# Kernel optimization log

Measured on AMD Instinct MI355X. Metric: run time of the kernel, lower is better.

Reference implementation:

```python
import jax, jax.numpy as jnp
import numpy as np

L = 8192   # sequence length
B = 4      # batch
D = 512    # embed_dim
NDIM = 16  # EMA state dim
Z = 128    # shared q/k dim
W = 128    # attention window
MP = 256   # max relative positions
NEG = -50000.0  # TOKEN_SELF_ATTN_VALUE-style mask fill


def setup_inputs() -> dict:
    key = jax.random.key(0)
    ks = jax.random.split(key, 16)
    def tn(k, shp, std):  # truncated-normal-ish init (clipped normal)
        return jnp.clip(jax.random.normal(k, shp) * std, -2 * std, 2 * std)
    val = jnp.ones((NDIM, 1)).at[1::2].set(-1.0)  # MultiHeadEMA beta init pattern
    return {
        "x": jax.random.normal(ks[0], (L, B, D), dtype=jnp.float32),
        "delta": tn(ks[1], (D, NDIM, 1), 0.2),
        "alpha": tn(ks[2], (D, NDIM, 1), 0.2),
        "beta": tn(ks[3], (D, NDIM, 1), 0.02) + val,
        "gamma": jax.random.normal(ks[4], (D, NDIM)),
        "omega": jax.random.normal(ks[5], (D,)),
        "Wp": tn(ks[6], (D, 1), 0.02),      # LatentConfigurator weight_proj
        "bp": jnp.zeros((1,)),
        "temp": jnp.array([0.5 * np.log(D)], dtype=jnp.float32),  # log(sqrt(D))
        "Wz": tn(ks[7], (D, Z), 0.02),
        "qg": jax.random.normal(ks[8], (Z,)) * 0.02 + 1.0,
        "qb": jnp.zeros((Z,)),
        "kg": jax.random.normal(ks[9], (Z,)) * 0.02 + 1.0,
        "kb": jnp.zeros((Z,)),
        "Wv": tn(ks[10], (D, D), 0.02),
        "relb": tn(ks[11], (2 * MP - 1,), 0.02),  # FastRelativePositionalBias table
    }


def _rotary(t, cos, sin):
    # t: (B, L, Z); cos/sin: (L, Z//2). Complex rotation on interleaved pairs.
    t1, t2 = t[..., 0::2], t[..., 1::2]
    return jnp.stack([t1 * cos - t2 * sin, t1 * sin + t2 * cos], axis=-1).reshape(t.shape)


def _forward(x, delta, alpha, beta, gamma, omega, Wp, bp, temp, Wz, qg, qb, kg, kb, Wv, relb):
    scale = 1.0 / np.sqrt(NDIM)
    # ---- MultiHeadEMA: damped EMA as long convolution via FFT ----
    p = jax.nn.sigmoid(delta)                      # (D,N,1)
    a = jax.nn.sigmoid(alpha)
    logq = jnp.log1p(-(p * a))                     # log(1 - p*alpha)
    t = jnp.arange(L, dtype=jnp.float32)
    kern = (p * beta) * jnp.exp(logq * t)          # (D,N,L) Vandermonde kernel
    k1d = jnp.einsum('dnl,dn->dl', kern, gamma * scale)  # (D,L)
    xb = x.transpose(1, 2, 0)                      # (B,D,L)
    conv = jnp.fft.irfft(jnp.fft.rfft(xb, n=2 * L) * jnp.fft.rfft(k1d, n=2 * L), n=2 * L)[..., :L]
    mx = jax.nn.silu(conv.transpose(2, 0, 1) + x * omega)  # (L,B,D)
    # ---- LatentConfigurator: sigmoid token routing (proj_dim==1) ----
    pi = jax.nn.sigmoid((mx @ Wp + bp) / jnp.exp(temp))[..., 0].T  # (B,L)
    mxb = mx.transpose(1, 0, 2)                    # (B,L,D)
    sel = pi > 0.5
    idx = jnp.cumsum(sel.astype(jnp.int32), axis=1) * sel  # (B,L); 0 -> dropped slot
    counts = sel.sum(axis=1)                       # (B,)
    bi = jnp.arange(B)[:, None]
    # compress_seq: scatter selected tokens to compact prefix (slot 0 dropped)
    c = jnp.zeros((B, L + 1, D), mx.dtype).at[bi, idx].add(mxb * sel[..., None])[:, 1:]
    # ---- windowed attention over compressed tokens ----
    z = jax.nn.silu(c @ Wz)                        # (B,L,Z)
    freqs = 1.0 / (10000.0 ** (jnp.arange(0, Z, 2, dtype=jnp.float32) / Z))
    ang = jnp.arange(L, dtype=jnp.float32)[:, None] * freqs
    cos, sin = jnp.cos(ang), jnp.sin(ang)
    q = _rotary(z * qg + qb, cos, sin)
    kk = _rotary(z * kg + kb, cos, sin)
    v = jax.nn.silu(c @ Wv)                        # (B,L,D)
    n = L // W
    qw = q.reshape(B, n, W, Z)
    def look_around(tw):  # prepend previous window: (B,n,W,f) -> (B,n,2W,f)
        prev = jnp.pad(tw, ((0, 0), (1, 0), (0, 0), (0, 0)))[:, :-1]
        return jnp.concatenate([prev, tw], axis=2)
    kw = look_around(kk.reshape(B, n, W, Z))
    vw = look_around(v.reshape(B, n, W, D))
    base = (jnp.arange(n) * W)[:, None, None]
    qabs = base + jnp.arange(W)[None, :, None]         # (n,W,1)
    kabs = base + jnp.arange(-W, W)[None, None, :]     # (n,1,2W)
    mask = (kabs <= qabs) & (kabs >= 0) & (kabs[None] < counts[:, None, None, None])  # (B,n,W,2W)
    rel = jnp.arange(-W, W)[None, :] - jnp.arange(W)[:, None]   # (W,2W)
    bias = relb[jnp.clip(rel + MP - 1, 0, 2 * MP - 2)]          # (W,2W)
    scores = jnp.einsum('bnwz,bnkz->bnwk', qw, kw) / np.sqrt(Z) + bias
    attn = jax.nn.softmax(jnp.where(mask, scores, NEG), axis=-1)
    h = jnp.einsum('bnwk,bnkd->bnwd', attn, vw).reshape(B, L, D)
    # ---- extract: gather back to original positions, gate by pi ----
    hpad = jnp.concatenate([jnp.zeros((B, 1, D), h.dtype), h], axis=1)
    hsel = jnp.take_along_axis(hpad, idx[..., None], axis=1)    # (B,L,D)
    return x + (hsel * pi[..., None]).transpose(1, 0, 2)        # (L,B,D)


def reference(x, delta, alpha, beta, gamma, omega, Wp, bp, temp, Wz, qg, qb, kg, kb, Wv, relb):
    return _forward(x, delta, alpha, beta, gamma, omega, Wp, bp, temp, Wz, qg, qb, kg, kb, Wv, relb)
```

## Files before the change

### kernel.cpp

```cpp
#include <hip/hip_runtime.h>
#include <math.h>

constexpr int L = 8192;
constexpr int B = 4;
constexpr int D = 512;
constexpr int NDIM = 16;
constexpr int Z = 128;
constexpr float NEGF = -50000.0f;
constexpr int CCL = 64;
constexpr int NCH = L / CCL;

typedef short s16x8 __attribute__((ext_vector_type(8)));
typedef float f32x4 __attribute__((ext_vector_type(4)));

typedef __attribute__((address_space(1))) const void* as1cv;
typedef __attribute__((address_space(3))) void* as3v;

__device__ __forceinline__ void gld16(const void* g, void* l) {
  __builtin_amdgcn_global_load_lds((as1cv)g, (as3v)l, 16, 0, 0);
}

__device__ __forceinline__ unsigned short f2bf(float f) {
  unsigned u = __builtin_bit_cast(unsigned, f);
  u += 0x7fffu + ((u >> 16) & 1u);
  return (unsigned short)(u >> 16);
}

__global__ __launch_bounds__(256) void k_prep(const float* __restrict__ delta,
                                              const float* __restrict__ alpha,
                                              const float* __restrict__ beta,
                                              const float* __restrict__ gamma,
                                              double* __restrict__ qdn,
                                              double* __restrict__ cdn,
                                              double* __restrict__ rp1,
                                              double* __restrict__ rp2) {
  int i = blockIdx.x * 256 + threadIdx.x;
  if (i >= D * NDIM) return;
  double p = 1.0 / (1.0 + exp(-(double)delta[i]));
  double a = 1.0 / (1.0 + exp(-(double)alpha[i]));
  double q = 1.0 - p * a;
  qdn[i] = q;
  cdn[i] = p * (double)beta[i] * (double)gamma[i] * 0.25;
  double q2 = q * q, q4 = q2 * q2, q8 = q4 * q4;
  double q16 = q8 * q8, q32 = q16 * q16, q64 = q32 * q32;
  rp1[i] = q64;
  rp2[i] = q64 * q64;
}

__global__ __launch_bounds__(256) void k_convA(const float* __restrict__ x,
                                               const double* __restrict__ qdn,
                                               float* __restrict__ E) {
  int bx = blockIdx.x;
  int tile = bx & 31, dg = (bx >> 5) & 7, b = bx >> 8;
  int d = threadIdx.x & 63, cl = threadIdx.x >> 6;
  int dgl = dg * 64 + d;
  int t = tile * 4 + cl;
  double q[NDIM], s[NDIM];
#pragma unroll
  for (int n = 0; n < NDIM; ++n) { q[n] = qdn[dgl * NDIM + n]; s[n] = 0.0; }
  const float* xp = x + ((size_t)(t * CCL) * B + b) * D + dgl;
#pragma unroll 4
  for (int i = 0; i < CCL; ++i) {
    double xv = (double)xp[(size_t)i * (B * D)];
#pragma unroll
    for (int n = 0; n < NDIM; ++n) s[n] = fma(q[n], s[n], xv);
  }
  float* eb = E + ((size_t)(b * NCH + t) * NDIM) * 512 + dgl;
#pragma unroll
  for (int n = 0; n < NDIM; ++n) eb[(size_t)n * 512] = (float)s[n];
}

__global__ __launch_bounds__(256) void k_convC(const float* __restrict__ x,
                                               const float* __restrict__ omega,
                                               const double* __restrict__ qdn,
                                               const double* __restrict__ cdn,
                                               const double* __restrict__ rp1,
                                               const double* __restrict__ rp2,
                                               const float* __restrict__ E,
                                               float* __restrict__ mx) {
  int bx = blockIdx.x;
  int tile = bx & 31, dg = (bx >> 5) & 7, b = bx >> 8;
  int d = threadIdx.x & 63, cl = threadIdx.x >> 6;
  int dgl = dg * 64 + d;
  int t = tile * 4 + cl;
  double q[NDIM], c[NDIM], s[NDIM];
#pragma unroll
  for (int n = 0; n < NDIM; ++n) {
    q[n] = qdn[dgl * NDIM + n];
    c[n] = cdn[dgl * NDIM + n];
    s[n] = 0.0;
  }
  if (t >= 1) {
    const float* e1 = E + ((size_t)(b * NCH + t - 1) * NDIM) * 512 + dgl;
#pragma unroll
    for (int n = 0; n < NDIM; ++n) s[n] = (double)e1[(size_t)n * 512];
  }
  if (t >= 2) {
    const float* e2 = E + ((size_t)(b * NCH + t - 2) * NDIM) * 512 + dgl;
#pragma unroll
    for (int n = 0; n < NDIM; ++n) s[n] = fma(rp1[dgl * NDIM + n], (double)e2[(size_t)n * 512], s[n]);
  }
  if (t >= 3) {
    const float* e3 = E + ((size_t)(b * NCH + t - 3) * NDIM) * 512 + dgl;
#pragma unroll
    for (int n = 0; n < NDIM; ++n) s[n] = fma(rp2[dgl * NDIM + n], (double)e3[(size_t)n * 512], s[n]);
  }
  double om = (double)omega[dgl];
  const float* xp = x + ((size_t)(t * CCL) * B + b) * D + dgl;
  float* mp = mx + ((size_t)b * L + t * CCL) * 512 + dgl;
#pragma unroll 4
  for (int i = 0; i < CCL; ++i) {
    double xv = (double)xp[(size_t)i * (B * D)];
#pragma unroll
    for (int n = 0; n < NDIM; ++n) s[n] = fma(q[n], s[n], xv);
    double p0 = c[0] * s[0], p1 = c[1] * s[1], p2 = c[2] * s[2], p3 = c[3] * s[3];
    p0 = fma(c[4], s[4], p0);  p1 = fma(c[5], s[5], p1);
    p2 = fma(c[6], s[6], p2);  p3 = fma(c[7], s[7], p3);
    p0 = fma(c[8], s[8], p0);  p1 = fma(c[9], s[9], p1);
    p2 = fma(c[10], s[10], p2); p3 = fma(c[11], s[11], p3);
    p0 = fma(c[12], s[12], p0); p1 = fma(c[13], s[13], p1);
    p2 = fma(c[14], s[14], p2); p3 = fma(c[15], s[15], p3);
    double conv = (p0 + p1) + (p2 + p3);
    float m = (float)(conv + xv * om);
    float sg = 1.0f / (1.0f + expf(-m));
    mp[(size_t)i * 512] = m * sg;
  }
}

__global__ __launch_bounds__(256) void k_logit(const float* __restrict__ mx,
                                               const float* __restrict__ Wp,
                                               const float* __restrict__ bp,
                                               const float* __restrict__ temp,
                                               float* __restrict__ pi,
                                               int* __restrict__ selb) {
  int rid = blockIdx.x * 4 + (threadIdx.x >> 6);
  int lane = threadIdx.x & 63;
  const float* row = mx + (size_t)rid * D;
  double acc = 0.0;
#pragma unroll
  for (int i = 0; i < D / 64; ++i)
    acc += (double)row[lane + 64 * i] * (double)Wp[lane + 64 * i];
  for (int off = 32; off; off >>= 1) acc += __shfl_down(acc, off, 64);
  if (lane == 0) {
    double logit = acc + (double)bp[0];
    double scl = logit / exp((double)temp[0]);
    pi[rid] = (float)(1.0 / (1.0 + exp(-scl)));
    selb[rid] = (logit > 0.0) ? 1 : 0;
  }
}

__global__ __launch_bounds__(256) void k_scan(const int* __restrict__ selb,
                                              int* __restrict__ idx,
                                              int* __restrict__ src,
                                              int* __restrict__ counts) {
  int b = blockIdx.x;
  int t = threadIdx.x;
  __shared__ int part[256];
  const int PER = L / 256;
  int base = b * L + t * PER;
  int loc[PER];
  int cnt = 0;
#pragma unroll
  for (int i = 0; i < PER; ++i) { loc[i] = selb[base + i]; cnt += loc[i]; }
  part[t] = cnt;
  __syncthreads();
  for (int off = 1; off < 256; off <<= 1) {
    int v = (t >= off) ? part[t - off] : 0;
    __syncthreads();
    part[t] += v;
    __syncthreads();
  }
  int run = (t == 0) ? 0 : part[t - 1];
#pragma unroll
  for (int i = 0; i < PER; ++i) {
    int sflag = loc[i];
    run += sflag;
    idx[base + i] = sflag ? run : 0;
    if (sflag) src[b * L + run - 1] = t * PER + i;
  }
  if (t == 255) counts[b] = part[255];
}

__global__ __launch_bounds__(256) void k_buildc(const float* __restrict__ mx,
                                                const int* __restrict__ src,
                                                const int* __restrict__ counts,
                                                unsigned short* __restrict__ c) {
  int row = blockIdx.x * 4 + (threadIdx.x >> 6);
  int lane = threadIdx.x & 63;
  int b = row >> 13;
  int j = row & (L - 1);
  float4 v0 = {0.f, 0.f, 0.f, 0.f}, v1 = v0;
  if (j < counts[b]) {
    const float4* mr = (const float4*)(mx + ((size_t)b * L + src[row]) * D);
    v0 = mr[lane * 2];
    v1 = mr[lane * 2 + 1];
  }
  s16x8 o;
  o[0] = (short)f2bf(v0.x); o[1] = (short)f2bf(v0.y);
  o[2] = (short)f2bf(v0.z); o[3] = (short)f2bf(v0.w);
  o[4] = (short)f2bf(v1.x); o[5] = (short)f2bf(v1.y);
  o[6] = (short)f2bf(v1.z); o[7] = (short)f2bf(v1.w);
  *(s16x8*)(c + (size_t)row * D + lane * 8) = o;
}

__global__ __launch_bounds__(256) void k_wt(const float* __restrict__ Wm,
                                            unsigned short* __restrict__ Wt, int N) {
  int idx = blockIdx.x * 256 + threadIdx.x;
  int n = idx >> 9, kk = idx & 511;
  Wt[idx] = f2bf(Wm[(size_t)kk * N + n]);
}

__global__ __launch_bounds__(256) void k_gemm_mfma(const unsigned short* __restrict__ A,
                                                   const unsigned short* __restrict__ Bt,
                                                   float* __restrict__ outF,
                                                   unsigned short* __restrict__ outT,
                                                   int N, int mode) {
  __shared__ char As[16384];
  __shared__ char Bs[16384];
  int tid = threadIdx.x;
  int w = tid >> 6, l = tid & 63;
  int m0 = blockIdx.x * 128, n0 = blockIdx.y * 128;
  int wr = w >> 1, wc = w & 1;
  f32x4 acc[4][4];
  f32x4 zz = {0.f, 0.f, 0.f, 0.f};
#pragma unroll
  for (int mi = 0; mi < 4; ++mi)
#pragma unroll
    for (int ni = 0; ni < 4; ++ni) acc[mi][ni] = zz;

  for (int k0 = 0; k0 < 512; k0 += 64) {
#pragma unroll
    for (int ld = 0; ld < 4; ++ld) {
      int li = w * 4 + ld;
      int row = li * 8 + (l >> 3);
      int col = (((l & 7) ^ (row & 7)) << 3);
      gld16(A + (size_t)(m0 + row) * 512 + k0 + col, As + li * 1024);
      gld16(Bt + (size_t)(n0 + row) * 512 + k0 + col, Bs + li * 1024);
    }
    __syncthreads();
    s16x8 af[4][2], bfr[4][2];
#pragma unroll
    for (int kh = 0; kh < 2; ++kh) {
#pragma unroll
      for (int mi = 0; mi < 4; ++mi) {
        int row = wr * 64 + mi * 16 + (l & 15);
        int byte = row * 128 + ((kh * 64 + ((l >> 4) * 16)) ^ ((row & 7) << 4));
        af[mi][kh] = *(const s16x8*)(As + byte);
      }
#pragma unroll
      for (int ni = 0; ni < 4; ++ni) {
        int row = wc * 64 + ni * 16 + (l & 15);
        int byte = row * 128 + ((kh * 64 + ((l >> 4) * 16)) ^ ((row & 7) << 4));
        bfr[ni][kh] = *(const s16x8*)(Bs + byte);
      }
    }
#pragma unroll
    for (int kh = 0; kh < 2; ++kh)
#pragma unroll
      for (int mi = 0; mi < 4; ++mi)
#pragma unroll
        for (int ni = 0; ni < 4; ++ni)
          acc[mi][ni] = __builtin_amdgcn_mfma_f32_16x16x32_bf16(af[mi][kh], bfr[ni][kh], acc[mi][ni], 0, 0, 0);
    __syncthreads();
  }
#pragma unroll
  for (int mi = 0; mi < 4; ++mi)
#pragma unroll
    for (int ni = 0; ni < 4; ++ni)
#pragma unroll
      for (int r = 0; r < 4; ++r) {
        float vv = acc[mi][ni][r];
        vv = vv / (1.0f + __expf(-vv));
        int mrow = m0 + wr * 64 + mi * 16 + (l >> 4) * 4 + r;
        int ncol = n0 + wc * 64 + ni * 16 + (l & 15);
        if (mode == 0) {
          outF[(size_t)mrow * N + ncol] = vv;
        } else {
          int b = mrow >> 13, j = mrow & 8191;
          outT[((size_t)(b * 512 + ncol)) * 8192 + j] = f2bf(vv);
        }
      }
}

__global__ __launch_bounds__(256) void k_rot(const float* __restrict__ z,
                                             const float* __restrict__ qg,
                                             const float* __restrict__ qb,
                                             const float* __restrict__ kg,
                                             const float* __restrict__ kb,
                                             unsigned short* __restrict__ qo,
                                             unsigned short* __restrict__ ko) {
  int tid = blockIdx.x * 256 + threadIdx.x;
  int i = tid & 63;
  int row = tid >> 6;
  int j = row & (L - 1);
  double freq = exp(((double)(-2 * i) / 128.0) * log(10000.0));
  float angf = (float)j * (float)freq;
  double sa, ca;
  sincos((double)angf, &sa, &ca);
  float cc = (float)ca, ss = (float)sa;
  size_t base = (size_t)row * Z + 2 * i;
  float z1 = z[base], z2 = z[base + 1];
  float q1 = z1 * qg[2 * i] + qb[2 * i], q2 = z2 * qg[2 * i + 1] + qb[2 * i + 1];
  float k1 = z1 * kg[2 * i] + kb[2 * i], k2 = z2 * kg[2 * i + 1] + kb[2 * i + 1];
  qo[base]     = f2bf(q1 * cc - q2 * ss);
  qo[base + 1] = f2bf(q1 * ss + q2 * cc);
  ko[base]     = f2bf(k1 * cc - k2 * ss);
  ko[base + 1] = f2bf(k1 * ss + k2 * cc);
}

__global__ __launch_bounds__(512) void k_attn_mfma(const unsigned short* __restrict__ q,
                                                   const unsigned short* __restrict__ k,
                                                   const unsigned short* __restrict__ vT,
                                                   const float* __restrict__ relb,
                                                   const int* __restrict__ counts,
                                                   float* __restrict__ h) {
  __shared__ char smem[131072];
  char* Qs = smem;
  char* Ks = smem + 32768;
  char* Ps = smem;
  char* Vs = smem + 65536;
  int tid = threadIdx.x, w = tid >> 6, l = tid & 63;
  int n = blockIdx.x & 63, b = blockIdx.x >> 6;
  int cnt = counts[b];
  int q0 = n * 128, kbase = q0 - 128;
  const size_t rowb = (size_t)b * L;

#pragma unroll
  for (int ld = 0; ld < 4; ++ld) {
    int li = w * 4 + ld;
    int row = li * 4 + (l >> 4);
    int colb = ((l & 15) * 16) ^ ((row & 7) << 4);
    gld16((const char*)(q + (rowb + q0 + row) * Z) + colb, Qs + li * 1024);
  }
#pragma unroll
  for (int ld = 0; ld < 8; ++ld) {
    int li = w * 8 + ld;
    int row = li * 4 + (l >> 4);
    int jk = kbase + row; if (jk < 0) jk = 0;
    int colb = ((l & 15) * 16) ^ ((row & 7) << 4);
    gld16((const char*)(k + (rowb + jk) * Z) + colb, Ks + li * 1024);
  }
  __syncthreads();

  int m0 = w * 16;
  f32x4 s[16];
  f32x4 zz = {0.f, 0.f, 0.f, 0.f};
#pragma unroll
  for (int ni = 0; ni < 16; ++ni) s[ni] = zz;
  s16x8 aq[4];
#pragma unroll
  for (int ks = 0; ks < 4; ++ks) {
    int row = m0 + (l & 15);
    int byte = row * 256 + ((ks * 64 + ((l >> 4) * 16)) ^ ((row & 7) << 4));
    aq[ks] = *(const s16x8*)(Qs + byte);
  }
#pragma unroll
  for (int ni = 0; ni < 16; ++ni) {
    int row = ni * 16 + (l & 15);
    int rb = row * 256, sw = (row & 7) << 4;
#pragma unroll
    for (int ks = 0; ks < 4; ++ks) {
      s16x8 bk = *(const s16x8*)(Ks + rb + ((ks * 64 + ((l >> 4) * 16)) ^ sw));
      s[ni] = __builtin_amdgcn_mfma_f32_16x16x32_bf16(aq[ks], bk, s[ni], 0, 0, 0);
    }
  }
  __syncthreads();

  auto stageV = [&](int nc) {
#pragma unroll
    for (int ld = 0; ld < 8; ++ld) {
      int li = w * 8 + ld;
      int row = li * 2 + (l >> 5);
      int colb = ((l & 31) * 16) ^ ((row & 7) << 4);
      int j = kbase + (colb >> 1);
      if (j < 0) j = 0;
      gld16((const char*)(vT + ((size_t)(b * 512 + nc * 128 + row)) * L + j), Vs + li * 1024);
    }
  };
  stageV(0);

  int rgrp = (l >> 4) * 4;
  float mxr[4] = {-3e38f, -3e38f, -3e38f, -3e38f};
#pragma unroll
  for (int ni = 0; ni < 16; ++ni) {
    int col = ni * 16 + (l & 15);
    int kabs = kbase + col;
#pragma unroll
    for (int r = 0; r < 4; ++r) {
      int ww = m0 + rgrp + r;
      bool valid = (kabs >= 0) && (kabs <= q0 + ww) && (kabs < cnt);
      float vv = valid ? (s[ni][r] * 0.08838834764831845f + relb[col + 127 - ww]) : NEGF;
      s[ni][r] = vv;
      mxr[r] = fmaxf(mxr[r], vv);
    }
  }
#pragma unroll
  for (int r = 0; r < 4; ++r)
    for (int off = 1; off < 16; off <<= 1)
      mxr[r] = fmaxf(mxr[r], __shfl_xor(mxr[r], off, 64));
  float smr[4] = {0.f, 0.f, 0.f, 0.f};
#pragma unroll
  for (int ni = 0; ni < 16; ++ni)
#pragma unroll
    for (int r = 0; r < 4; ++r) {
      float p = __expf(s[ni][r] - mxr[r]);
      s[ni][r] = p;
      smr[r] += p;
    }
#pragma unroll
  for (int r = 0; r < 4; ++r) {
    for (int off = 1; off < 16; off <<= 1) smr[r] += __shfl_xor(smr[r], off, 64);
    smr[r] = 1.0f / smr[r];
  }
#pragma unroll
  for (int ni = 0; ni < 16; ++ni) {
    int colb2 = (ni * 16 + (l & 15)) * 2;
#pragma unroll
    for (int r = 0; r < 4; ++r) {
      int row = m0 + rgrp + r;
      *(unsigned short*)(Ps + row * 512 + (colb2 ^ ((row & 7) << 4))) = f2bf(s[ni][r] * smr[r]);
    }
  }
  __syncthreads();

  for (int nc = 0; nc < 4; ++nc) {
    if (nc) {
      __syncthreads();
      stageV(nc);
      __syncthreads();
    }
    f32x4 o[8];
#pragma unroll
    for (int ni = 0; ni < 8; ++ni) o[ni] = zz;
    int prow = m0 + (l & 15);
    int psw = (prow & 7) << 4;
#pragma unroll
    for (int kt = 0; kt < 4; ++kt) {
      s16x8 pa0 = *(const s16x8*)(Ps + prow * 512 + ((kt * 128 + ((l >> 4) * 16)) ^ psw));
      s16x8 pa1 = *(const s16x8*)(Ps + prow * 512 + ((kt * 128 + 64 + ((l >> 4) * 16)) ^ psw));
#pragma unroll
      for (int ni = 0; ni < 8; ++ni) {
        int vrow = ni * 16 + (l & 15);
        int vsw = (vrow & 7) << 4;
        s16x8 vb0 = *(const s16x8*)(Vs + vrow * 512 + ((kt * 128 + ((l >> 4) * 16)) ^ vsw));
        s16x8 vb1 = *(const s16x8*)(Vs + vrow * 512 + ((kt * 128 + 64 + ((l >> 4) * 16)) ^ vsw));
        o[ni] = __builtin_amdgcn_mfma_f32_16x16x32_bf16(pa0, vb0, o[ni], 0, 0, 0);
        o[ni] = __builtin_amdgcn_mfma_f32_16x16x32_bf16(pa1, vb1, o[ni], 0, 0, 0);
      }
    }
#pragma unroll
    for (int ni = 0; ni < 8; ++ni)
#pragma unroll
      for (int r = 0; r < 4; ++r)
        h[(rowb + q0 + m0 + rgrp + r) * 512 + nc * 128 + ni * 16 + (l & 15)] = o[ni][r];
  }
}

__global__ __launch_bounds__(256) void k_final(const float* __restrict__ x,
                                               const float* __restrict__ h,
                                               const float* __restrict__ pi,
                                               const int* __restrict__ idx,
                                               float* __restrict__ out) {
  int e4 = blockIdx.x * 256 + threadIdx.x;
  int dq = e4 & 127;
  int rem = e4 >> 7;
  int b = rem & 3;
  int l = rem >> 2;
  float4 xv = ((const float4*)x)[e4];
  int ix = idx[(b << 13) + l];
  if (ix > 0) {
    float pv = pi[(b << 13) + l];
    float4 hv = ((const float4*)(h + ((size_t)(b << 13) + ix - 1) * 512))[dq];
    xv.x += hv.x * pv; xv.y += hv.y * pv;
    xv.z += hv.z * pv; xv.w += hv.w * pv;
  }
  ((float4*)out)[e4] = xv;
}

extern "C" void kernel_launch(void* const* d_in, const int* in_sizes, int n_in,
                              void* d_out, int out_size, void* d_ws, size_t ws_size,
                              hipStream_t stream) {
  const float* x     = (const float*)d_in[0];
  const float* delta = (const float*)d_in[1];
  const float* alpha = (const float*)d_in[2];
  const float* beta  = (const float*)d_in[3];
  const float* gamma = (const float*)d_in[4];
  const float* omega = (const float*)d_in[5];
  const float* Wp    = (const float*)d_in[6];
  const float* bp    = (const float*)d_in[7];
  const float* temp  = (const float*)d_in[8];
  const float* Wz    = (const float*)d_in[9];
  const float* qg    = (const float*)d_in[10];
  const float* qb    = (const float*)d_in[11];
  const float* kg    = (const float*)d_in[12];
  const float* kb    = (const float*)d_in[13];
  const float* Wv    = (const float*)d_in[14];
  const float* relb  = (const float*)d_in[15];
  (void)in_sizes; (void)n_in; (void)out_size; (void)ws_size;

  char* wsb = (char*)d_ws;
  size_t o = 0;
  auto alloc = [&](size_t bytes) {
    char* p = wsb + o;
    o += (bytes + 255) & ~(size_t)255;
    return p;
  };
  float* mxv           = (float*)alloc((size_t)B * L * D * 4);
  char*  eAndCb        = alloc((size_t)B * L * D * 2);
  float* Ebuf          = (float*)eAndCb;
  unsigned short* cb   = (unsigned short*)eAndCb;
  float* zb            = (float*)alloc((size_t)B * L * Z * 4);
  unsigned short* qb2  = (unsigned short*)alloc((size_t)B * L * Z * 2);
  unsigned short* kb2  = (unsigned short*)alloc((size_t)B * L * Z * 2);
  unsigned short* vTb  = (unsigned short*)alloc((size_t)B * D * L * 2);
  unsigned short* wzt  = (unsigned short*)alloc((size_t)Z * 512 * 2);
  unsigned short* wvt  = (unsigned short*)alloc((size_t)D * 512 * 2);
  float* pib = (float*)alloc((size_t)B * L * 4);
  int* selb  = (int*)alloc((size_t)B * L * 4);
  int* idx   = (int*)alloc((size_t)B * L * 4);
  int* src   = (int*)alloc((size_t)B * L * 4);
  int* cnt   = (int*)alloc(256);
  double* qdn = (double*)alloc((size_t)D * NDIM * 8);
  double* cdn = (double*)alloc((size_t)D * NDIM * 8);
  double* rp1 = (double*)alloc((size_t)D * NDIM * 8);
  double* rp2 = (double*)alloc((size_t)D * NDIM * 8);

  k_prep<<<(D * NDIM + 255) / 256, 256, 0, stream>>>(delta, alpha, beta, gamma, qdn, cdn, rp1, rp2);
  k_convA<<<B * 8 * 32, 256, 0, stream>>>(x, qdn, Ebuf);
  k_convC<<<B * 8 * 32, 256, 0, stream>>>(x, omega, qdn, cdn, rp1, rp2, Ebuf, mxv);
  k_logit<<<B * L / 4, 256, 0, stream>>>(mxv, Wp, bp, temp, pib, selb);
  k_scan<<<B, 256, 0, stream>>>(selb, idx, src, cnt);
  k_buildc<<<B * L / 4, 256, 0, stream>>>(mxv, src, cnt, cb);
  k_wt<<<Z * 512 / 256, 256, 0, stream>>>(Wz, wzt, Z);
  k_wt<<<D * 512 / 256, 256, 0, stream>>>(Wv, wvt, D);
  k_gemm_mfma<<<dim3(256, 1), 256, 0, stream>>>(cb, wzt, zb, vTb, Z, 0);
  k_gemm_mfma<<<dim3(256, 4), 256, 0, stream>>>(cb, wvt, zb, vTb, D, 1);
  k_rot<<<B * L * (Z / 2) / 256, 256, 0, stream>>>(zb, qg, qb, kg, kb, qb2, kb2);
  k_attn_mfma<<<B * 64, 512, 0, stream>>>(qb2, kb2, vTb, relb, cnt, mxv);
  k_final<<<(int)((size_t)L * B * D / 4 / 256), 256, 0, stream>>>(x, mxv, pib, idx, (float*)d_out);
}
```

Baseline: 270.5 us.

## Run EMA convolution in fp32, fuse logit dot, store bf16 mx, fix near-zero logits

The EMA chunked convolution moves from double to single precision, and the Wp projection dot product is fused into the convolution kernel through per-64-channel partial sums. This drops the separate logit pass over the fp32 mx buffer, and mx is now written as bf16, so buildc only gathers rows. Rows whose logit lands near zero are flagged and recomputed in double precision by small fix kernels, to keep the selection decision faithful. The cost is two extra tiny launches, an atomic counter, and reduced precision in the pi values and in mx.

```diff
diff --git a/kernel.cpp b/kernel.cpp
--- a/kernel.cpp
+++ b/kernel.cpp
@@ -9,6 +9,7 @@
 constexpr float NEGF = -50000.0f;
 constexpr int CCL = 64;
 constexpr int NCH = L / CCL;
+constexpr int FMAX = 64;
 
 typedef short s16x8 __attribute__((ext_vector_type(8)));
 typedef float f32x4 __attribute__((ext_vector_type(4)));
@@ -33,120 +34,212 @@
                                               double* __restrict__ qdn,
                                               double* __restrict__ cdn,
                                               double* __restrict__ rp1,
-                                              double* __restrict__ rp2) {
+                                              double* __restrict__ rp2,
+                                              float* __restrict__ qf,
+                                              float* __restrict__ cf,
+                                              float* __restrict__ r1f,
+                                              float* __restrict__ r2f,
+                                              int* __restrict__ fcnt) {
   int i = blockIdx.x * 256 + threadIdx.x;
+  if (i == 0) *fcnt = 0;
   if (i >= D * NDIM) return;
   double p = 1.0 / (1.0 + exp(-(double)delta[i]));
   double a = 1.0 / (1.0 + exp(-(double)alpha[i]));
   double q = 1.0 - p * a;
-  qdn[i] = q;
-  cdn[i] = p * (double)beta[i] * (double)gamma[i] * 0.25;
+  double c = p * (double)beta[i] * (double)gamma[i] * 0.25;
+  qdn[i] = q; cdn[i] = c;
   double q2 = q * q, q4 = q2 * q2, q8 = q4 * q4;
   double q16 = q8 * q8, q32 = q16 * q16, q64 = q32 * q32;
   rp1[i] = q64;
   rp2[i] = q64 * q64;
+  qf[i] = (float)q; cf[i] = (float)c;
+  r1f[i] = (float)q64; r2f[i] = (float)(q64 * q64);
 }
 
 __global__ __launch_bounds__(256) void k_convA(const float* __restrict__ x,
-                                               const double* __restrict__ qdn,
+                                               const float* __restrict__ qf,
                                                float* __restrict__ E) {
   int bx = blockIdx.x;
   int tile = bx & 31, dg = (bx >> 5) & 7, b = bx >> 8;
-  int d = threadIdx.x & 63, cl = threadIdx.x >> 6;
-  int dgl = dg * 64 + d;
+  int dl = threadIdx.x & 63, cl = threadIdx.x >> 6;
+  int dgl = dg * 64 + dl;
   int t = tile * 4 + cl;
-  double q[NDIM], s[NDIM];
-#pragma unroll
-  for (int n = 0; n < NDIM; ++n) { q[n] = qdn[dgl * NDIM + n]; s[n] = 0.0; }
+  float q[NDIM], s[NDIM];
+#pragma unroll
+  for (int n = 0; n < NDIM; ++n) { q[n] = qf[dgl * NDIM + n]; s[n] = 0.f; }
   const float* xp = x + ((size_t)(t * CCL) * B + b) * D + dgl;
 #pragma unroll 4
   for (int i = 0; i < CCL; ++i) {
-    double xv = (double)xp[(size_t)i * (B * D)];
-#pragma unroll
-    for (int n = 0; n < NDIM; ++n) s[n] = fma(q[n], s[n], xv);
+    float xv = xp[i * (B * D)];
+#pragma unroll
+    for (int n = 0; n < NDIM; ++n) s[n] = fmaf(q[n], s[n], xv);
   }
   float* eb = E + ((size_t)(b * NCH + t) * NDIM) * 512 + dgl;
 #pragma unroll
-  for (int n = 0; n < NDIM; ++n) eb[(size_t)n * 512] = (float)s[n];
+  for (int n = 0; n < NDIM; ++n) eb[(size_t)n * 512] = s[n];
 }
 
 __global__ __launch_bounds__(256) void k_convC(const float* __restrict__ x,
                                                const float* __restrict__ omega,
-                                               const double* __restrict__ qdn,
-                                               const double* __restrict__ cdn,
-                                               const double* __restrict__ rp1,
-                                               const double* __restrict__ rp2,
+                                               const float* __restrict__ qf,
+                                               const float* __restrict__ cf,
+                                               const float* __restrict__ r1f,
+                                               const float* __restrict__ r2f,
                                                const float* __restrict__ E,
-                                               float* __restrict__ mx) {
+                                               const float* __restrict__ Wp,
+                                               unsigned short* __restrict__ mxb,
+                                               float* __restrict__ pdot) {
   int bx = blockIdx.x;
   int tile = bx & 31, dg = (bx >> 5) & 7, b = bx >> 8;
-  int d = threadIdx.x & 63, cl = threadIdx.x >> 6;
-  int dgl = dg * 64 + d;
+  int dl = threadIdx.x & 63, cl = threadIdx.x >> 6;
+  int dgl = dg * 64 + dl;
   int t = tile * 4 + cl;
-  double q[NDIM], c[NDIM], s[NDIM];
+  float q[NDIM], c[NDIM], s[NDIM];
 #pragma unroll
   for (int n = 0; n < NDIM; ++n) {
-    q[n] = qdn[dgl * NDIM + n];
-    c[n] = cdn[dgl * NDIM + n];
-    s[n] = 0.0;
+    q[n] = qf[dgl * NDIM + n];
+    c[n] = cf[dgl * NDIM + n];
+    s[n] = 0.f;
   }
   if (t >= 1) {
     const float* e1 = E + ((size_t)(b * NCH + t - 1) * NDIM) * 512 + dgl;
 #pragma unroll
-    for (int n = 0; n < NDIM; ++n) s[n] = (double)e1[(size_t)n * 512];
+    for (int n = 0; n < NDIM; ++n) s[n] = e1[(size_t)n * 512];
   }
   if (t >= 2) {
     const float* e2 = E + ((size_t)(b * NCH + t - 2) * NDIM) * 512 + dgl;
 #pragma unroll
-    for (int n = 0; n < NDIM; ++n) s[n] = fma(rp1[dgl * NDIM + n], (double)e2[(size_t)n * 512], s[n]);
+    for (int n = 0; n < NDIM; ++n) s[n] = fmaf(r1f[dgl * NDIM + n], e2[(size_t)n * 512], s[n]);
   }
   if (t >= 3) {
     const float* e3 = E + ((size_t)(b * NCH + t - 3) * NDIM) * 512 + dgl;
 #pragma unroll
-    for (int n = 0; n < NDIM; ++n) s[n] = fma(rp2[dgl * NDIM + n], (double)e3[(size_t)n * 512], s[n]);
-  }
-  double om = (double)omega[dgl];
+    for (int n = 0; n < NDIM; ++n) s[n] = fmaf(r2f[dgl * NDIM + n], e3[(size_t)n * 512], s[n]);
+  }
+  float om = omega[dgl];
+  float wp = Wp[dgl];
   const float* xp = x + ((size_t)(t * CCL) * B + b) * D + dgl;
-  float* mp = mx + ((size_t)b * L + t * CCL) * 512 + dgl;
-#pragma unroll 4
+  unsigned short* mp = mxb + ((size_t)b * L + t * CCL) * 512 + dgl;
+  float* pp = pdot + ((size_t)(b * L + t * CCL)) * 8 + dg;
   for (int i = 0; i < CCL; ++i) {
-    double xv = (double)xp[(size_t)i * (B * D)];
-#pragma unroll
-    for (int n = 0; n < NDIM; ++n) s[n] = fma(q[n], s[n], xv);
-    double p0 = c[0] * s[0], p1 = c[1] * s[1], p2 = c[2] * s[2], p3 = c[3] * s[3];
-    p0 = fma(c[4], s[4], p0);  p1 = fma(c[5], s[5], p1);
-    p2 = fma(c[6], s[6], p2);  p3 = fma(c[7], s[7], p3);
-    p0 = fma(c[8], s[8], p0);  p1 = fma(c[9], s[9], p1);
-    p2 = fma(c[10], s[10], p2); p3 = fma(c[11], s[11], p3);
-    p0 = fma(c[12], s[12], p0); p1 = fma(c[13], s[13], p1);
-    p2 = fma(c[14], s[14], p2); p3 = fma(c[15], s[15], p3);
-    double conv = (p0 + p1) + (p2 + p3);
-    float m = (float)(conv + xv * om);
-    float sg = 1.0f / (1.0f + expf(-m));
-    mp[(size_t)i * 512] = m * sg;
-  }
-}
-
-__global__ __launch_bounds__(256) void k_logit(const float* __restrict__ mx,
-                                               const float* __restrict__ Wp,
-                                               const float* __restrict__ bp,
-                                               const float* __restrict__ temp,
-                                               float* __restrict__ pi,
-                                               int* __restrict__ selb) {
-  int rid = blockIdx.x * 4 + (threadIdx.x >> 6);
-  int lane = threadIdx.x & 63;
-  const float* row = mx + (size_t)rid * D;
+    float xv = xp[i * (B * D)];
+#pragma unroll
+    for (int n = 0; n < NDIM; ++n) s[n] = fmaf(q[n], s[n], xv);
+    float p0 = c[0] * s[0], p1 = c[1] * s[1], p2 = c[2] * s[2], p3 = c[3] * s[3];
+    p0 = fmaf(c[4], s[4], p0);  p1 = fmaf(c[5], s[5], p1);
+    p2 = fmaf(c[6], s[6], p2);  p3 = fmaf(c[7], s[7], p3);
+    p0 = fmaf(c[8], s[8], p0);  p1 = fmaf(c[9], s[9], p1);
+    p2 = fmaf(c[10], s[10], p2); p3 = fmaf(c[11], s[11], p3);
+    p0 = fmaf(c[12], s[12], p0); p1 = fmaf(c[13], s[13], p1);
+    p2 = fmaf(c[14], s[14], p2); p3 = fmaf(c[15], s[15], p3);
+    float conv = (p0 + p1) + (p2 + p3);
+    float m = fmaf(xv, om, conv);
+    float v = m / (1.0f + __expf(-m));
+    mp[(size_t)i * 512] = f2bf(v);
+    float pd = v * wp;
+#pragma unroll
+    for (int off = 32; off; off >>= 1) pd += __shfl_down(pd, off, 64);
+    if (dl == 0) pp[(size_t)i * 8] = pd;
+  }
+}
+
+__global__ __launch_bounds__(256) void k_logitc(const float* __restrict__ pdot,
+                                                const float* __restrict__ bp,
+                                                const float* __restrict__ temp,
+                                                float* __restrict__ pi,
+                                                int* __restrict__ selb,
+                                                int* __restrict__ fcnt,
+                                                int* __restrict__ flags) {
+  int rid = blockIdx.x * 256 + threadIdx.x;
+  const float* pr = pdot + (size_t)rid * 8;
   double acc = 0.0;
 #pragma unroll
-  for (int i = 0; i < D / 64; ++i)
-    acc += (double)row[lane + 64 * i] * (double)Wp[lane + 64 * i];
-  for (int off = 32; off; off >>= 1) acc += __shfl_down(acc, off, 64);
-  if (lane == 0) {
-    double logit = acc + (double)bp[0];
-    double scl = logit / exp((double)temp[0]);
-    pi[rid] = (float)(1.0 / (1.0 + exp(-scl)));
-    selb[rid] = (logit > 0.0) ? 1 : 0;
-  }
+  for (int j = 0; j < 8; ++j) acc += (double)pr[j];
+  double logit = acc + (double)bp[0];
+  pi[rid] = (float)(1.0 / (1.0 + exp(-logit / exp((double)temp[0]))));
+  selb[rid] = (logit > 0.0) ? 1 : 0;
+  if (fabs(logit) < 1e-4) {
+    int slot = atomicAdd(fcnt, 1);
+    if (slot < FMAX) flags[slot] = rid;
+  }
+}
+
+__global__ __launch_bounds__(256) void k_fix(const int* __restrict__ fcnt,
+                                             const int* __restrict__ flags,
+                                             const float* __restrict__ x,
+                                             const double* __restrict__ qdn,
+                                             const double* __restrict__ cdn,
+                                             const double* __restrict__ rp1,
+                                             const double* __restrict__ rp2,
+                                             const float* __restrict__ omega,
+                                             const float* __restrict__ Wp,
+                                             double* __restrict__ pfix) {
+  int nb = blockIdx.x;
+  int fi = nb >> 3, dblk = nb & 7;
+  int count = *fcnt; if (count > FMAX) count = FMAX;
+  if (fi >= count) return;
+  int rid = flags[fi];
+  int b = rid >> 13, l = rid & (L - 1);
+  int t = l >> 6, io = l & 63;
+  int sub = threadIdx.x >> 6, dl = threadIdx.x & 63;
+  int d = dblk * 64 + dl;
+  double q[NDIM], s[NDIM];
+#pragma unroll
+  for (int n = 0; n < NDIM; ++n) { q[n] = qdn[d * NDIM + n]; s[n] = 0.0; }
+  int c0 = (sub < 3) ? (t - 3 + sub) : t;
+  int steps = (sub < 3) ? 64 : (io + 1);
+  if (c0 >= 0) {
+    const float* xp = x + ((size_t)(c0 * CCL) * B + b) * D + d;
+    for (int i = 0; i < steps; ++i) {
+      double xv = (double)xp[(size_t)i * (B * D)];
+#pragma unroll
+      for (int n = 0; n < NDIM; ++n) s[n] = fma(q[n], s[n], xv);
+    }
+  }
+  __shared__ double Esm[4][64][NDIM];
+#pragma unroll
+  for (int n = 0; n < NDIM; ++n) Esm[sub][dl][n] = s[n];
+  __syncthreads();
+  if (sub == 3) {
+    double sfin[NDIM];
+#pragma unroll
+    for (int n = 0; n < NDIM; ++n) {
+      double base = q[n], r = 1.0;
+      int e = io + 1;
+      while (e) { if (e & 1) r *= base; base *= base; e >>= 1; }
+      double S = Esm[2][dl][n] + rp1[d * NDIM + n] * Esm[1][dl][n] + rp2[d * NDIM + n] * Esm[0][dl][n];
+      sfin[n] = Esm[3][dl][n] + r * S;
+    }
+    double conv = 0.0;
+#pragma unroll
+    for (int n = 0; n < NDIM; ++n) conv = fma(cdn[d * NDIM + n], sfin[n], conv);
+    double xv = (double)x[((size_t)l * B + b) * D + d];
+    double m = conv + xv * (double)omega[d];
+    double mxd = m / (1.0 + exp(-m));
+    double v = mxd * (double)Wp[d];
+#pragma unroll
+    for (int off = 32; off; off >>= 1) v += __shfl_down(v, off, 64);
+    if (dl == 0) pfix[fi * 8 + dblk] = v;
+  }
+}
+
+__global__ __launch_bounds__(64) void k_fix2(const int* __restrict__ fcnt,
+                                             const int* __restrict__ flags,
+                                             const double* __restrict__ pfix,
+                                             const float* __restrict__ bp,
+                                             const float* __restrict__ temp,
+                                             float* __restrict__ pi,
+                                             int* __restrict__ selb) {
+  int fi = threadIdx.x;
+  int count = *fcnt; if (count > FMAX) count = FMAX;
+  if (fi >= count) return;
+  double s = 0.0;
+#pragma unroll
+  for (int j = 0; j < 8; ++j) s += pfix[fi * 8 + j];
+  double logit = s + (double)bp[0];
+  int rid = flags[fi];
+  selb[rid] = (logit > 0.0) ? 1 : 0;
+  pi[rid] = (float)(1.0 / (1.0 + exp(-logit / exp((double)temp[0]))));
 }
 
 __global__ __launch_bounds__(256) void k_scan(const int* __restrict__ selb,
@@ -181,7 +274,7 @@
   if (t == 255) counts[b] = part[255];
 }
 
-__global__ __launch_bounds__(256) void k_buildc(const float* __restrict__ mx,
+__global__ __launch_bounds__(256) void k_buildc(const unsigned short* __restrict__ mxb,
                                                 const int* __restrict__ src,
                                                 const int* __restrict__ counts,
                                                 unsigned short* __restrict__ c) {
@@ -189,17 +282,9 @@
   int lane = threadIdx.x & 63;
   int b = row >> 13;
   int j = row & (L - 1);
-  float4 v0 = {0.f, 0.f, 0.f, 0.f}, v1 = v0;
-  if (j < counts[b]) {
-    const float4* mr = (const float4*)(mx + ((size_t)b * L + src[row]) * D);
-    v0 = mr[lane * 2];
-    v1 = mr[lane * 2 + 1];
-  }
-  s16x8 o;
-  o[0] = (short)f2bf(v0.x); o[1] = (short)f2bf(v0.y);
-  o[2] = (short)f2bf(v0.z); o[3] = (short)f2bf(v0.w);
-  o[4] = (short)f2bf(v1.x); o[5] = (short)f2bf(v1.y);
-  o[6] = (short)f2bf(v1.z); o[7] = (short)f2bf(v1.w);
+  s16x8 o = {0, 0, 0, 0, 0, 0, 0, 0};
+  if (j < counts[b])
+    o = *(const s16x8*)(mxb + ((size_t)b * L + src[row]) * 512 + lane * 8);
   *(s16x8*)(c + (size_t)row * D + lane * 8) = o;
 }
 
@@ -505,7 +590,8 @@
     o += (bytes + 255) & ~(size_t)255;
     return p;
   };
-  float* mxv           = (float*)alloc((size_t)B * L * D * 4);
+  float* hbuf          = (float*)alloc((size_t)B * L * D * 4);
+  unsigned short* mxb  = (unsigned short*)hbuf;
   char*  eAndCb        = alloc((size_t)B * L * D * 2);
   float* Ebuf          = (float*)eAndCb;
   unsigned short* cb   = (unsigned short*)eAndCb;
@@ -515,27 +601,38 @@
   unsigned short* vTb  = (unsigned short*)alloc((size_t)B * D * L * 2);
   unsigned short* wzt  = (unsigned short*)alloc((size_t)Z * 512 * 2);
   unsigned short* wvt  = (unsigned short*)alloc((size_t)D * 512 * 2);
-  float* pib = (float*)alloc((size_t)B * L * 4);
-  int* selb  = (int*)alloc((size_t)B * L * 4);
-  int* idx   = (int*)alloc((size_t)B * L * 4);
-  int* src   = (int*)alloc((size_t)B * L * 4);
-  int* cnt   = (int*)alloc(256);
+  float* pdot = (float*)alloc((size_t)B * L * 8 * 4);
+  float* pib  = (float*)alloc((size_t)B * L * 4);
+  int* selb   = (int*)alloc((size_t)B * L * 4);
+  int* idx    = (int*)alloc((size_t)B * L * 4);
+  int* src    = (int*)alloc((size_t)B * L * 4);
+  int* cnt    = (int*)alloc(256);
   double* qdn = (double*)alloc((size_t)D * NDIM * 8);
   double* cdn = (double*)alloc((size_t)D * NDIM * 8);
   double* rp1 = (double*)alloc((size_t)D * NDIM * 8);
   double* rp2 = (double*)alloc((size_t)D * NDIM * 8);
-
-  k_prep<<<(D * NDIM + 255) / 256, 256, 0, stream>>>(delta, alpha, beta, gamma, qdn, cdn, rp1, rp2);
-  k_convA<<<B * 8 * 32, 256, 0, stream>>>(x, qdn, Ebuf);
-  k_convC<<<B * 8 * 32, 256, 0, stream>>>(x, omega, qdn, cdn, rp1, rp2, Ebuf, mxv);
-  k_logit<<<B * L / 4, 256, 0, stream>>>(mxv, Wp, bp, temp, pib, selb);
+  float* qf   = (float*)alloc((size_t)D * NDIM * 4);
+  float* cf   = (float*)alloc((size_t)D * NDIM * 4);
+  float* r1f  = (float*)alloc((size_t)D * NDIM * 4);
+  float* r2f  = (float*)alloc((size_t)D * NDIM * 4);
+  int* fcnt   = (int*)alloc(256);
+  int* flags  = (int*)alloc(FMAX * 4);
+  double* pfix = (double*)alloc((size_t)FMAX * 8 * 8);
+
+  k_prep<<<(D * NDIM + 255) / 256, 256, 0, stream>>>(delta, alpha, beta, gamma,
+                                                     qdn, cdn, rp1, rp2, qf, cf, r1f, r2f, fcnt);
+  k_convA<<<B * 8 * 32, 256, 0, stream>>>(x, qf, Ebuf);
+  k_convC<<<B * 8 * 32, 256, 0, stream>>>(x, omega, qf, cf, r1f, r2f, Ebuf, Wp, mxb, pdot);
+  k_logitc<<<B * L / 256, 256, 0, stream>>>(pdot, bp, temp, pib, selb, fcnt, flags);
+  k_fix<<<FMAX * 8, 256, 0, stream>>>(fcnt, flags, x, qdn, cdn, rp1, rp2, omega, Wp, pfix);
+  k_fix2<<<1, 64, 0, stream>>>(fcnt, flags, pfix, bp, temp, pib, selb);
   k_scan<<<B, 256, 0, stream>>>(selb, idx, src, cnt);
-  k_buildc<<<B * L / 4, 256, 0, stream>>>(mxv, src, cnt, cb);
+  k_buildc<<<B * L / 4, 256, 0, stream>>>(mxb, src, cnt, cb);
   k_wt<<<Z * 512 / 256, 256, 0, stream>>>(Wz, wzt, Z);
   k_wt<<<D * 512 / 256, 256, 0, stream>>>(Wv, wvt, D);
   k_gemm_mfma<<<dim3(256, 1), 256, 0, stream>>>(cb, wzt, zb, vTb, Z, 0);
   k_gemm_mfma<<<dim3(256, 4), 256, 0, stream>>>(cb, wvt, zb, vTb, D, 1);
   k_rot<<<B * L * (Z / 2) / 256, 256, 0, stream>>>(zb, qg, qb, kg, kb, qb2, kb2);
-  k_attn_mfma<<<B * 64, 512, 0, stream>>>(qb2, kb2, vTb, relb, cnt, mxv);
-  k_final<<<(int)((size_t)L * B * D / 4 / 256), 256, 0, stream>>>(x, mxv, pib, idx, (float*)d_out);
-}
+  k_attn_mfma<<<B * 64, 512, 0, stream>>>(qb2, kb2, vTb, relb, cnt, hbuf);
+  k_final<<<(int)((size_t)L * B * D / 4 / 256), 256, 0, stream>>>(x, hbuf, pib, idx, (float*)d_out);
+}
```

After: 272.2 us. Within noise of the previous version (+0.7%).
